# Kernel optimization log

Measured on AMD Instinct MI355X. Metric: run time of the kernel, lower is better.

Reference implementation:

```python
import jax, jax.numpy as jnp
import numpy as np


def setup_inputs() -> dict:
    key = jax.random.key(0)
    k1, k2 = jax.random.split(key)
    N, C = 65536, 2048
    features = jax.random.normal(k1, (N, C), dtype=jnp.float32)
    pids = jax.random.randint(k2, (N,), 0, 751, dtype=jnp.int32)
    return {"features": features, "pids": pids}


def reference(features, pids):
    # Sum each consecutive group of 4 rows: (N, C) -> (N//4, 4, C) -> (N//4, C)
    N, C = features.shape
    chunk = N // 4
    integrating_features = features.reshape(chunk, 4, C).sum(axis=1)
    # Original casts pids to int32 via torch.int
    integrating_pids = pids[::4].astype(jnp.int32)
    return integrating_features, integrating_pids
```

## Files before the change

kernel.cpp:

```cpp
#include <hip/hip_runtime.h>
#include <hip/hip_bf16.h>


__global__ void feat_group4_sum_kernel(const float4* __restrict__ in,
                                       float4* __restrict__ out_feat,
                                       const int* __restrict__ pids,
                                       float* __restrict__ out_pids,
                                       int c4,
                                       int total_v4)
{
    const int stride = gridDim.x * blockDim.x;
    for (int i = blockIdx.x * blockDim.x + threadIdx.x; i < total_v4; i += stride) {
        const int g = i / c4;
        const int c = i - g * c4;
        const float4* __restrict__ base = in + (size_t)g * 4 * c4 + c;
        float4 a = base[0];
        float4 b = base[c4];
        float4 d = base[2 * c4];
        float4 e = base[3 * c4];
        float4 s;
        s.x = (a.x + b.x) + (d.x + e.x);
        s.y = (a.y + b.y) + (d.y + e.y);
        s.z = (a.z + b.z) + (d.z + e.z);
        s.w = (a.w + b.w) + (d.w + e.w);
        out_feat[i] = s;
        if (c == 0) {
            out_pids[g] = (float)pids[(size_t)g * 4];
        }
    }
}

extern "C" void kernel_launch(void* const* d_in, const int* in_sizes, int n_in,
                              void* d_out, int out_size, void* d_ws, size_t ws_size,
                              hipStream_t stream) {
    const float* features = (const float*)d_in[0];
    const int*   pids     = (const int*)d_in[1];

    const int N = in_sizes[1];
    const int C = in_sizes[0] / N;
    const int G = N / 4;
    const int c4 = C / 4;
    const int total_v4 = G * c4;

    float* out_feat_f = (float*)d_out;
    float* out_pids_f = out_feat_f + (size_t)G * C;

    const int block = 256;
    int grid = (total_v4 + block - 1) / block;
    if (grid > 8192) grid = 8192;

    feat_group4_sum_kernel<<<grid, block, 0, stream>>>(
        (const float4*)features, (float4*)out_feat_f, pids, out_pids_f,
        c4, total_v4);
}
```

Measured before the change: 133.9 us.

## Use 2D grid with nontemporal loads/stores and split pid gather kernel

Replaces the grid-stride loop with a 2D launch where each block handles one group row, which removes the per-element integer division. Feature loads and stores use nontemporal builtins to avoid polluting the cache on this streaming workload. The pid gather moves into a separate small kernel, which adds a second launch in exchange for a branch-free main kernel.

Measured after the change: 114.7 us. 14.3% less time.

```diff
diff --git a/kernel.cpp b/kernel.cpp
--- a/kernel.cpp
+++ b/kernel.cpp
@@ -2,31 +2,32 @@
 #include <hip/hip_bf16.h>
 
 
-__global__ void feat_group4_sum_kernel(const float4* __restrict__ in,
-                                       float4* __restrict__ out_feat,
-                                       const int* __restrict__ pids,
-                                       float* __restrict__ out_pids,
-                                       int c4,
-                                       int total_v4)
+typedef float f32x4 __attribute__((ext_vector_type(4)));
+
+__global__ void feat_group4_sum_kernel(const f32x4* __restrict__ in,
+                                       f32x4* __restrict__ out_feat,
+                                       int c4)
 {
-    const int stride = gridDim.x * blockDim.x;
-    for (int i = blockIdx.x * blockDim.x + threadIdx.x; i < total_v4; i += stride) {
-        const int g = i / c4;
-        const int c = i - g * c4;
-        const float4* __restrict__ base = in + (size_t)g * 4 * c4 + c;
-        float4 a = base[0];
-        float4 b = base[c4];
-        float4 d = base[2 * c4];
-        float4 e = base[3 * c4];
-        float4 s;
-        s.x = (a.x + b.x) + (d.x + e.x);
-        s.y = (a.y + b.y) + (d.y + e.y);
-        s.z = (a.z + b.z) + (d.z + e.z);
-        s.w = (a.w + b.w) + (d.w + e.w);
-        out_feat[i] = s;
-        if (c == 0) {
-            out_pids[g] = (float)pids[(size_t)g * 4];
-        }
+    const int c = blockIdx.x * blockDim.x + threadIdx.x;
+    const int g = blockIdx.y;
+    if (c >= c4) return;
+
+    const f32x4* __restrict__ base = in + (size_t)g * 4 * c4 + c;
+    f32x4 a = __builtin_nontemporal_load(base);
+    f32x4 b = __builtin_nontemporal_load(base + c4);
+    f32x4 d = __builtin_nontemporal_load(base + 2 * c4);
+    f32x4 e = __builtin_nontemporal_load(base + 3 * c4);
+    f32x4 s = (a + b) + (d + e);
+    __builtin_nontemporal_store(s, out_feat + (size_t)g * c4 + c);
+}
+
+__global__ void pids_gather_kernel(const int* __restrict__ pids,
+                                   float* __restrict__ out_pids,
+                                   int G)
+{
+    const int g = blockIdx.x * blockDim.x + threadIdx.x;
+    if (g < G) {
+        out_pids[g] = (float)pids[(size_t)g * 4];
     }
 }
 
@@ -40,16 +41,15 @@
     const int C = in_sizes[0] / N;
     const int G = N / 4;
     const int c4 = C / 4;
-    const int total_v4 = G * c4;
 
     float* out_feat_f = (float*)d_out;
     float* out_pids_f = out_feat_f + (size_t)G * C;
 
     const int block = 256;
-    int grid = (total_v4 + block - 1) / block;
-    if (grid > 8192) grid = 8192;
+    dim3 grid((c4 + block - 1) / block, G, 1);
+    feat_group4_sum_kernel<<<grid, block, 0, stream>>>(
+        (const f32x4*)features, (f32x4*)out_feat_f, c4);
 
-    feat_group4_sum_kernel<<<grid, block, 0, stream>>>(
-        (const float4*)features, (float4*)out_feat_f, pids, out_pids_f,
-        c4, total_v4);
+    pids_gather_kernel<<<(G + block - 1) / block, block, 0, stream>>>(
+        pids, out_pids_f, G);
 }
```
